# Kernel tuning notes

Hardware: AMD Instinct MI355X
Metric: run time of the kernel (lower is better)

Reference implementation:

```python
import jax, jax.numpy as jnp
import numpy as np

B = 8192          # batch rows
F0 = 2048         # base input features
E = 512           # embed rows added per recursion level
L = 3             # chain depth
OUT = 2048        # MAIN output dim
NNZ_E = 8192      # nnz per embed sparse weight (~16/row)
NNZ_M = 16384     # nnz of MAIN sparse weight (~8/row)


def _spmm_t(rows, cols, vals, x, n_rows):
    """Compute (W_sparse @ x.T).T = x @ W.T for COO W of shape [n_rows, x.shape[1]].
    out[b, r] = sum_{k: rows[k]==r} vals[k] * x[b, cols[k]]
    """
    contrib = x[:, cols] * vals                     # [B, nnz]
    return jax.ops.segment_sum(contrib.T, rows, num_segments=n_rows).T  # [B, n_rows]


def setup_inputs() -> dict:
    key = jax.random.key(0)
    ks = jax.random.split(key, 12)
    widths = [F0, F0 + E, F0 + 2 * E]               # input width at each recursion level
    inp = {"x": jax.random.normal(ks[0], (B, F0), dtype=jnp.float32)}
    for i, w in enumerate(widths):
        inp[f"emb_rows{i}"] = jax.random.randint(ks[1 + 3 * i], (NNZ_E,), 0, E, dtype=jnp.int32)
        inp[f"emb_cols{i}"] = jax.random.randint(ks[2 + 3 * i], (NNZ_E,), 0, w, dtype=jnp.int32)
        inp[f"emb_vals{i}"] = jax.random.normal(ks[3 + 3 * i], (NNZ_E,), dtype=jnp.float32)
    inp["main_rows"] = jax.random.randint(ks[10], (NNZ_M,), 0, OUT, dtype=jnp.int32)
    inp["main_cols"] = jax.random.randint(ks[11], (NNZ_M,), 0, F0 + 3 * E, dtype=jnp.int32)
    inp["main_vals"] = jax.random.normal(jax.random.fold_in(key, 99), (NNZ_M,), dtype=jnp.float32)
    return inp


def reference(x, emb_rows0, emb_cols0, emb_vals0,
              emb_rows1, emb_cols1, emb_vals1,
              emb_rows2, emb_cols2, emb_vals2,
              main_rows, main_cols, main_vals):
    # Recursive chain unrolled oldest-first: each level sparse-mms its embed
    # weight against the running input and concatenates the result.
    h = x
    for rows, cols, vals in ((emb_rows0, emb_cols0, emb_vals0),
                             (emb_rows1, emb_cols1, emb_vals1),
                             (emb_rows2, emb_cols2, emb_vals2)):
        e = _spmm_t(rows, cols, vals, h, E)         # [B, E]
        h = jnp.concatenate([h, e], axis=1)
    # is_last: pass concatenated features through the MAIN sparse linear
    return _spmm_t(main_rows, main_cols, main_vals, h, OUT)  # [B, OUT]
```

## Files before the change

kernel.cpp:

```cpp
#include <hip/hip_runtime.h>
#include <stdint.h>

#define F0    2048
#define EROWS 512
#define NOUT  2048
#define MROWS 8192

typedef __attribute__((ext_vector_type(8))) short bf16x8;
typedef __attribute__((ext_vector_type(4))) float f32x4;
typedef __attribute__((ext_vector_type(8))) unsigned short u16x8;

typedef const __attribute__((address_space(1))) unsigned char ga_t;
typedef __attribute__((address_space(3))) unsigned char lds_t;

__device__ __forceinline__ void async_load16(const void* g, void* l) {
  __builtin_amdgcn_global_load_lds((ga_t*)g, (lds_t*)l, 16, 0, 0);
}

__device__ __forceinline__ unsigned short f2bf(float f) {
  unsigned int u = __builtin_bit_cast(unsigned int, f);
  u += 0x7fffu + ((u >> 16) & 1u);
  return (unsigned short)(u >> 16);
}

__global__ __launch_bounds__(256) void csr_cast_kernel(
    const int* __restrict__ r0, const int* __restrict__ c0, const float* __restrict__ v0, int n0,
    const int* __restrict__ r1, const int* __restrict__ c1, const float* __restrict__ v1, int n1,
    const int* __restrict__ r2, const int* __restrict__ c2, const float* __restrict__ v2, int n2,
    const int* __restrict__ rm, const int* __restrict__ cm, const float* __restrict__ vm, int nm,
    int* __restrict__ rp_all, int* __restrict__ cc_all, float* __restrict__ cv_all)
{
  const int b = blockIdx.x;
  const int tid = threadIdx.x;

  const int* rows; const int* cols; const float* vals; int nnz, nrows;
  if      (b == 0) { rows = r0; cols = c0; vals = v0; nnz = n0; nrows = EROWS; }
  else if (b == 1) { rows = r1; cols = c1; vals = v1; nnz = n1; nrows = EROWS; }
  else if (b == 2) { rows = r2; cols = c2; vals = v2; nnz = n2; nrows = EROWS; }
  else             { rows = rm; cols = cm; vals = vm; nnz = nm; nrows = NOUT; }
  int* rp  = rp_all + b * 4096;
  int* cc  = cc_all + b * 8192;
  float* cv = cv_all + b * 8192;

  __shared__ int hist[NOUT + 1];
  __shared__ int tsum[256];

  for (int i = tid; i < nrows; i += 256) hist[i] = 0;
  __syncthreads();

  int k0 = 0;
  for (; k0 + 2048 <= nnz; k0 += 2048) {
    const int kk = k0 + tid * 8;
    int4 ra = *(const int4*)(rows + kk);
    int4 rb = *(const int4*)(rows + kk + 4);
    atomicAdd(&hist[ra.x], 1); atomicAdd(&hist[ra.y], 1);
    atomicAdd(&hist[ra.z], 1); atomicAdd(&hist[ra.w], 1);
    atomicAdd(&hist[rb.x], 1); atomicAdd(&hist[rb.y], 1);
    atomicAdd(&hist[rb.z], 1); atomicAdd(&hist[rb.w], 1);
  }
  for (int k = k0 + tid; k < nnz; k += 256) atomicAdd(&hist[rows[k]], 1);
  __syncthreads();

  const int per = nrows >> 8;
  const int base = tid * per;
  int sum = 0;
  for (int i = 0; i < per; ++i) sum += hist[base + i];
  tsum[tid] = sum;
  __syncthreads();
  for (int off = 1; off < 256; off <<= 1) {
    int add = (tid >= off) ? tsum[tid - off] : 0;
    __syncthreads();
    tsum[tid] += add;
    __syncthreads();
  }
  int run = (tid == 0) ? 0 : tsum[tid - 1];
  for (int i = 0; i < per; ++i) { int h = hist[base + i]; hist[base + i] = run; run += h; }
  __syncthreads();

  for (int i = tid; i < nrows; i += 256) rp[i] = hist[i];
  if (tid == 0) rp[nrows] = nnz;
  __syncthreads();

  k0 = 0;
  for (; k0 + 2048 <= nnz; k0 += 2048) {
    const int kk = k0 + tid * 8;
    int4   ra = *(const int4*)(rows + kk);
    int4   rb = *(const int4*)(rows + kk + 4);
    int4   ca = *(const int4*)(cols + kk);
    int4   cb2 = *(const int4*)(cols + kk + 4);
    float4 va = *(const float4*)(vals + kk);
    float4 vb = *(const float4*)(vals + kk + 4);
    int p;
    p = atomicAdd(&hist[ra.x], 1); cc[p] = ca.x;  cv[p] = va.x;
    p = atomicAdd(&hist[ra.y], 1); cc[p] = ca.y;  cv[p] = va.y;
    p = atomicAdd(&hist[ra.z], 1); cc[p] = ca.z;  cv[p] = va.z;
    p = atomicAdd(&hist[ra.w], 1); cc[p] = ca.w;  cv[p] = va.w;
    p = atomicAdd(&hist[rb.x], 1); cc[p] = cb2.x; cv[p] = vb.x;
    p = atomicAdd(&hist[rb.y], 1); cc[p] = cb2.y; cv[p] = vb.y;
    p = atomicAdd(&hist[rb.z], 1); cc[p] = cb2.z; cv[p] = vb.z;
    p = atomicAdd(&hist[rb.w], 1); cc[p] = cb2.w; cv[p] = vb.w;
  }
  for (int k = k0 + tid; k < nnz; k += 256) {
    int p = atomicAdd(&hist[rows[k]], 1);
    cc[p] = cols[k]; cv[p] = vals[k];
  }
}

template <bool BF16OUT>
__global__ __launch_bounds__(256) void expand_csr_kernel(
    const int* __restrict__ rp, const int* __restrict__ cc,
    const float* __restrict__ cv, const float* __restrict__ Dsrc,
    void* __restrict__ out, int nrows,
    const float* __restrict__ x, unsigned short* __restrict__ Ab, int cast_base)
{
  const int b = blockIdx.x;
  const int tid = threadIdx.x;

  if (b >= nrows) {
    const int cb = cast_base + (b - nrows);
    const float4* xp = (const float4*)x;
    u16x8* ap = (u16x8*)Ab;
#pragma unroll
    for (int it = 0; it < 4; ++it) {
      int i = cb * 1024 + it * 256 + tid;
      float4 a = xp[2 * i], c = xp[2 * i + 1];
      u16x8 o;
      o[0] = f2bf(a.x); o[1] = f2bf(a.y); o[2] = f2bf(a.z); o[3] = f2bf(a.w);
      o[4] = f2bf(c.x); o[5] = f2bf(c.y); o[6] = f2bf(c.z); o[7] = f2bf(c.w);
      ap[i] = o;
    }
    return;
  }

  const int r = b;
  __shared__ float acc[F0];
  __shared__ int   icol[128];
  __shared__ float ival[128];
  __shared__ int   icnt;

  float4* a4 = (float4*)acc;
  a4[tid * 2]     = (float4){0.f, 0.f, 0.f, 0.f};
  a4[tid * 2 + 1] = (float4){0.f, 0.f, 0.f, 0.f};
  if (tid == 0) icnt = 0;
  __syncthreads();

  const int s = rp[r], e = rp[r + 1];
  for (int i = s + tid; i < e; i += 256) {
    int c = cc[i]; float v = cv[i];
    if (c < F0) atomicAdd(&acc[c], v);
    else { int p = atomicAdd(&icnt, 1); if (p < 128) { icol[p] = c - F0; ival[p] = v; } }
  }
  __syncthreads();
  int n = icnt; if (n > 128) n = 128;

  float4 q0 = a4[tid * 2], q1 = a4[tid * 2 + 1];
  for (int j = 0; j < n; ++j) {
    const float4* src = (const float4*)(Dsrc + (size_t)icol[j] * F0) + tid * 2;
    float v = ival[j];
    float4 s0 = src[0], s1 = src[1];
    q0.x += v * s0.x; q0.y += v * s0.y; q0.z += v * s0.z; q0.w += v * s0.w;
    q1.x += v * s1.x; q1.y += v * s1.y; q1.z += v * s1.z; q1.w += v * s1.w;
  }

  if (BF16OUT) {
    u16x8 o;
    o[0] = f2bf(q0.x); o[1] = f2bf(q0.y); o[2] = f2bf(q0.z); o[3] = f2bf(q0.w);
    o[4] = f2bf(q1.x); o[5] = f2bf(q1.y); o[6] = f2bf(q1.z); o[7] = f2bf(q1.w);
    ((u16x8*)out)[(size_t)r * 256 + tid] = o;
  } else {
    float4* dst = (float4*)out + (size_t)r * 512 + tid * 2;
    dst[0] = q0; dst[1] = q1;
  }
}

__global__ __launch_bounds__(512, 2) void gemm256_kernel(
    const unsigned short* __restrict__ A, const unsigned short* __restrict__ B,
    float* __restrict__ C)
{
  constexpr int K  = F0;
  constexpr int N  = NOUT;
  constexpr int NT = K / 64;

  extern __shared__ __align__(16) unsigned short lds[];
  unsigned short* sA = lds;
  unsigned short* sB = lds + 32768;

  const int tid  = threadIdx.x;
  const int lane = tid & 63;
  const int w    = tid >> 6;
  const int wr   = w >> 2;
  const int wc   = w & 3;
  const int mm   = lane & 15;
  const int g    = lane >> 4;
  const int sx   = mm & 7;
  const int bm   = blockIdx.y;
  const int bn   = blockIdx.x;

  const unsigned short* Ag = A + (size_t)bm * 256 * K;
  const unsigned short* Bg = B + (size_t)bn * 256 * K;

  const int    r0    = tid >> 3;
  const int    c0    = (tid & 7) ^ (r0 & 7);
  const size_t goff0 = (size_t)r0 * K + c0 * 8;
  const size_t goff1 = goff0 + (size_t)64 * K;
  const int    loff0 = tid * 8;
  const int    loff1 = 4096 + tid * 8;

#define STG(Gb, Sb, buf, h, t) do {                                           \
    async_load16((Gb) + goff0 + (size_t)(h) * 128 * K + (t) * 64,             \
                 (Sb) + (buf) * 16384 + (h) * 8192 + loff0);                  \
    async_load16((Gb) + goff1 + (size_t)(h) * 128 * K + (t) * 64,             \
                 (Sb) + (buf) * 16384 + (h) * 8192 + loff1);                  \
  } while (0)

  const unsigned short* paB = sA + (wr * 128 + mm) * 64;
  const unsigned short* pbB = sB + (wc * 64  + mm) * 64;
  const int s0 = ((0 * 4 + g) ^ sx) * 8;
  const int s1 = ((1 * 4 + g) ^ sx) * 8;

  bf16x8 afP[4][2];
  bf16x8 afQ[4][2];
  bf16x8 bf0[2][2];
  bf16x8 bf1[2][2];

#define LDA(dst, buf, qm) do {                                                \
    const unsigned short* p_ = paB + (buf) * 16384 + (qm) * 4096;             \
    _Pragma("unroll") for (int tm = 0; tm < 4; ++tm) {                        \
      dst[tm][0] = *(const bf16x8*)(p_ + tm * 1024 + s0);                     \
      dst[tm][1] = *(const bf16x8*)(p_ + tm * 1024 + s1);                     \
    } } while (0)

#define LDB(dst, buf, qn) do {                                                \
    const unsigned short* p_ = pbB + (buf) * 16384 + (qn) * 2048;             \
    _Pragma("unroll") for (int tn = 0; tn < 2; ++tn) {                        \
      dst[tn][0] = *(const bf16x8*)(p_ + tn * 1024 + s0);                     \
      dst[tn][1] = *(const bf16x8*)(p_ + tn * 1024 + s1);                     \
    } } while (0)

#define MFMA_Q(qm, qn, afX, bfX) do {                                         \
    __builtin_amdgcn_s_setprio(1);                                            \
    _Pragma("unroll") for (int tm = 0; tm < 4; ++tm)                          \
    _Pragma("unroll") for (int tn = 0; tn < 2; ++tn) {                        \
      acc[(qm)*4+tm][(qn)*2+tn] = __builtin_amdgcn_mfma_f32_16x16x32_bf16(    \
          afX[tm][0], bfX[tn][0], acc[(qm)*4+tm][(qn)*2+tn], 0, 0, 0);        \
      acc[(qm)*4+tm][(qn)*2+tn] = __builtin_amdgcn_mfma_f32_16x16x32_bf16(    \
          afX[tm][1], bfX[tn][1], acc[(qm)*4+tm][(qn)*2+tn], 0, 0, 0);        \
    }                                                                         \
    __builtin_amdgcn_s_setprio(0);                                            \
  } while (0)

#define CFENCE     asm volatile("" ::: "memory")
#define BAR        do { CFENCE; __builtin_amdgcn_s_barrier(); CFENCE; } while (0)
#define SCHED0     __builtin_amdgcn_sched_barrier(0)
#define WAIT_VM(n) asm volatile("s_waitcnt vmcnt(" #n ")" ::: "memory")

  f32x4 acc[8][4];
#pragma unroll
  for (int i = 0; i < 8; ++i)
#pragma unroll
    for (int j = 0; j < 4; ++j) acc[i][j] = (f32x4)0.f;

  STG(Bg, sB, 0, 0, 0);
  STG(Bg, sB, 0, 1, 0);
  STG(Ag, sA, 0, 0, 0);
  STG(Ag, sA, 0, 1, 0);
  STG(Bg, sB, 1, 0, 1);
  STG(Bg, sB, 1, 1, 1);
  STG(Ag, sA, 1, 0, 1);
  WAIT_VM(6);
  BAR;
  SCHED0;
  LDA(afP, 0, 0);
  LDB(bf0, 0, 0);

#pragma unroll 2
  for (int t = 0; t < NT; ++t) {
    const int buf  = t & 1;
    const int nbuf = buf ^ 1;

    if (t + 1 < NT) STG(Ag, sA, nbuf, 1, t + 1);
    if (t + 1 < NT) { WAIT_VM(8); } else { WAIT_VM(0); }
    SCHED0;
    LDB(bf1, buf, 1);
    MFMA_Q(0, 0, afP, bf0);

    BAR; SCHED0;
    LDA(afQ, buf, 1);
    MFMA_Q(0, 1, afP, bf1);

    BAR;
    if (t + 2 < NT) STG(Bg, sB, buf, 0, t + 2);
    MFMA_Q(1, 0, afQ, bf0);

    BAR;
    if (t + 2 < NT) {
      STG(Bg, sB, buf, 1, t + 2);
      STG(Ag, sA, buf, 0, t + 2);
      WAIT_VM(6);
      BAR; SCHED0;
      LDA(afP, nbuf, 0);
      LDB(bf0, nbuf, 0);
    } else if (t + 1 < NT) {
      WAIT_VM(0);
      BAR; SCHED0;
      LDA(afP, nbuf, 0);
      LDB(bf0, nbuf, 0);
    }
    MFMA_Q(1, 1, afQ, bf1);
  }

  const int rowb = bm * 256 + wr * 128 + g * 4;
  const int colb = bn * 256 + wc * 64 + mm;
#pragma unroll
  for (int im = 0; im < 8; ++im) {
#pragma unroll
    for (int in2 = 0; in2 < 4; ++in2) {
      const int row = rowb + im * 16;
      const int col = colb + in2 * 16;
#pragma unroll
      for (int r = 0; r < 4; ++r)
        C[(size_t)(row + r) * N + col] = acc[im][in2][r];
    }
  }

#undef STG
#undef LDA
#undef LDB
#undef MFMA_Q
#undef CFENCE
#undef BAR
#undef SCHED0
#undef WAIT_VM
}

extern "C" void kernel_launch(void* const* d_in, const int* in_sizes, int n_in,
                              void* d_out, int out_size, void* d_ws, size_t ws_size,
                              hipStream_t stream)
{
  const float* x   = (const float*)d_in[0];
  const int*   er0 = (const int*)d_in[1];
  const int*   ec0 = (const int*)d_in[2];
  const float* ev0 = (const float*)d_in[3];
  const int*   er1 = (const int*)d_in[4];
  const int*   ec1 = (const int*)d_in[5];
  const float* ev1 = (const float*)d_in[6];
  const int*   er2 = (const int*)d_in[7];
  const int*   ec2 = (const int*)d_in[8];
  const float* ev2 = (const float*)d_in[9];
  const int*   mr  = (const int*)d_in[10];
  const int*   mc  = (const int*)d_in[11];
  const float* mv  = (const float*)d_in[12];
  const int nnz_e0 = in_sizes[1];
  const int nnz_e1 = in_sizes[4];
  const int nnz_e2 = in_sizes[7];
  const int nnz_m  = in_sizes[10];

  int*   rp_all = (int*)d_ws;
  int*   cc_all = rp_all + 4 * 4096;
  float* cv_all = (float*)(cc_all + 48 * 1024);
  float* D      = (float*)(cv_all + 48 * 1024);
  unsigned short* Mb = (unsigned short*)(D + (size_t)3 * EROWS * F0);
  unsigned short* Ab = Mb + (size_t)NOUT * F0;

  hipLaunchKernelGGL(csr_cast_kernel, dim3(4), dim3(256), 0, stream,
                     er0, ec0, ev0, nnz_e0,
                     er1, ec1, ev1, nnz_e1,
                     er2, ec2, ev2, nnz_e2,
                     mr,  mc,  mv,  nnz_m,
                     rp_all, cc_all, cv_all);

  hipLaunchKernelGGL((expand_csr_kernel<false>), dim3(EROWS + 512), dim3(256), 0, stream,
                     rp_all + 0 * 4096, cc_all + 0 * 8192, cv_all + 0 * 8192,
                     D, (void*)D, EROWS, x, Ab, 0);
  hipLaunchKernelGGL((expand_csr_kernel<false>), dim3(EROWS + 512), dim3(256), 0, stream,
                     rp_all + 1 * 4096, cc_all + 1 * 8192, cv_all + 1 * 8192,
                     D, (void*)(D + (size_t)EROWS * F0), EROWS, x, Ab, 512);
  hipLaunchKernelGGL((expand_csr_kernel<false>), dim3(EROWS + 512), dim3(256), 0, stream,
                     rp_all + 2 * 4096, cc_all + 2 * 8192, cv_all + 2 * 8192,
                     D, (void*)(D + (size_t)2 * EROWS * F0), EROWS, x, Ab, 1024);
  hipLaunchKernelGGL((expand_csr_kernel<true>), dim3(NOUT + 512), dim3(256), 0, stream,
                     rp_all + 3 * 4096, cc_all + 3 * 8192, cv_all + 3 * 8192,
                     D, (void*)Mb, NOUT, x, Ab, 1536);

  hipFuncSetAttribute(reinterpret_cast<const void*>(gemm256_kernel),
                      hipFuncAttributeMaxDynamicSharedMemorySize, 131072);
  hipLaunchKernelGGL(gemm256_kernel, dim3(NOUT / 256, MROWS / 256), dim3(512),
                     131072, stream, Ab, Mb, (float*)d_out);
}
```

Measured before the change: 237.3 us.

## Collapse embed chain expansion into a single worklist-driven tree expansion kernel

Replaces the three sequential per-level dense embed-matrix expansions plus the main expansion with one kernel. Each main row walks its references to embed rows through a shared-memory worklist and accumulates directly into the F0-wide row. The x-to-bf16 cast moves into the CSR build kernel, and the GEMM block order is remapped for cache locality. This removes three launches and the D intermediate traffic. The cost is serial worklist processing with a barrier per entry, and a 2048-entry cap that could truncate deep fan-out.

Result: slower. 262.9 us (+10.8%).

```diff
diff --git a/kernel.cpp b/kernel.cpp
--- a/kernel.cpp
+++ b/kernel.cpp
@@ -28,10 +28,27 @@
     const int* __restrict__ r1, const int* __restrict__ c1, const float* __restrict__ v1, int n1,
     const int* __restrict__ r2, const int* __restrict__ c2, const float* __restrict__ v2, int n2,
     const int* __restrict__ rm, const int* __restrict__ cm, const float* __restrict__ vm, int nm,
-    int* __restrict__ rp_all, int* __restrict__ cc_all, float* __restrict__ cv_all)
+    int* __restrict__ rp_all, int* __restrict__ cc_all, float* __restrict__ cv_all,
+    const float* __restrict__ x, unsigned short* __restrict__ Ab)
 {
   const int b = blockIdx.x;
   const int tid = threadIdx.x;
+
+  if (b >= 4) {
+    const int cb = b - 4;
+    const float4* xp = (const float4*)x;
+    u16x8* ap = (u16x8*)Ab;
+#pragma unroll
+    for (int it = 0; it < 4; ++it) {
+      int i = cb * 1024 + it * 256 + tid;
+      float4 a = xp[2 * i], c = xp[2 * i + 1];
+      u16x8 o;
+      o[0] = f2bf(a.x); o[1] = f2bf(a.y); o[2] = f2bf(a.z); o[3] = f2bf(a.w);
+      o[4] = f2bf(c.x); o[5] = f2bf(c.y); o[6] = f2bf(c.z); o[7] = f2bf(c.w);
+      ap[i] = o;
+    }
+    return;
+  }
 
   const int* rows; const int* cols; const float* vals; int nnz, nrows;
   if      (b == 0) { rows = r0; cols = c0; vals = v0; nnz = n0; nrows = EROWS; }
@@ -106,71 +123,62 @@
   }
 }
 
-template <bool BF16OUT>
-__global__ __launch_bounds__(256) void expand_csr_kernel(
-    const int* __restrict__ rp, const int* __restrict__ cc,
-    const float* __restrict__ cv, const float* __restrict__ Dsrc,
-    void* __restrict__ out, int nrows,
-    const float* __restrict__ x, unsigned short* __restrict__ Ab, int cast_base)
+__global__ __launch_bounds__(256) void expand_tree_kernel(
+    const int* __restrict__ rp_all, const int* __restrict__ cc_all,
+    const float* __restrict__ cv_all, unsigned short* __restrict__ Mb)
 {
-  const int b = blockIdx.x;
+  const int r = blockIdx.x;
   const int tid = threadIdx.x;
-
-  if (b >= nrows) {
-    const int cb = cast_base + (b - nrows);
-    const float4* xp = (const float4*)x;
-    u16x8* ap = (u16x8*)Ab;
-#pragma unroll
-    for (int it = 0; it < 4; ++it) {
-      int i = cb * 1024 + it * 256 + tid;
-      float4 a = xp[2 * i], c = xp[2 * i + 1];
-      u16x8 o;
-      o[0] = f2bf(a.x); o[1] = f2bf(a.y); o[2] = f2bf(a.z); o[3] = f2bf(a.w);
-      o[4] = f2bf(c.x); o[5] = f2bf(c.y); o[6] = f2bf(c.z); o[7] = f2bf(c.w);
-      ap[i] = o;
-    }
-    return;
-  }
-
-  const int r = b;
   __shared__ float acc[F0];
-  __shared__ int   icol[128];
-  __shared__ float ival[128];
-  __shared__ int   icnt;
+  __shared__ int   wl_row[2048];
+  __shared__ float wl_sc[2048];
+  __shared__ int   wl_n;
+  __shared__ int   wl_snap;
 
   float4* a4 = (float4*)acc;
   a4[tid * 2]     = (float4){0.f, 0.f, 0.f, 0.f};
   a4[tid * 2 + 1] = (float4){0.f, 0.f, 0.f, 0.f};
-  if (tid == 0) icnt = 0;
-  __syncthreads();
-
-  const int s = rp[r], e = rp[r + 1];
-  for (int i = s + tid; i < e; i += 256) {
-    int c = cc[i]; float v = cv[i];
-    if (c < F0) atomicAdd(&acc[c], v);
-    else { int p = atomicAdd(&icnt, 1); if (p < 128) { icol[p] = c - F0; ival[p] = v; } }
-  }
-  __syncthreads();
-  int n = icnt; if (n > 128) n = 128;
-
-  float4 q0 = a4[tid * 2], q1 = a4[tid * 2 + 1];
-  for (int j = 0; j < n; ++j) {
-    const float4* src = (const float4*)(Dsrc + (size_t)icol[j] * F0) + tid * 2;
-    float v = ival[j];
-    float4 s0 = src[0], s1 = src[1];
-    q0.x += v * s0.x; q0.y += v * s0.y; q0.z += v * s0.z; q0.w += v * s0.w;
-    q1.x += v * s1.x; q1.y += v * s1.y; q1.z += v * s1.z; q1.w += v * s1.w;
-  }
-
-  if (BF16OUT) {
-    u16x8 o;
-    o[0] = f2bf(q0.x); o[1] = f2bf(q0.y); o[2] = f2bf(q0.z); o[3] = f2bf(q0.w);
-    o[4] = f2bf(q1.x); o[5] = f2bf(q1.y); o[6] = f2bf(q1.z); o[7] = f2bf(q1.w);
-    ((u16x8*)out)[(size_t)r * 256 + tid] = o;
-  } else {
-    float4* dst = (float4*)out + (size_t)r * 512 + tid * 2;
-    dst[0] = q0; dst[1] = q1;
-  }
+  if (tid == 0) wl_n = 0;
+  __syncthreads();
+
+  {
+    const int* rp3 = rp_all + 3 * 4096;
+    const int s = rp3[r], e = rp3[r + 1];
+    for (int i = s + tid; i < e; i += 256) {
+      int c = cc_all[3 * 8192 + i]; float v = cv_all[3 * 8192 + i];
+      if (c < F0) atomicAdd(&acc[c], v);
+      else { int p = atomicAdd(&wl_n, 1); if (p < 2048) { wl_row[p] = c - F0; wl_sc[p] = v; } }
+    }
+  }
+  __syncthreads();
+
+  int pos = 0;
+  while (true) {
+    if (tid == 0) wl_snap = wl_n;
+    __syncthreads();
+    int nn = wl_snap;
+    if (nn > 2048) nn = 2048;
+    if (pos >= nn) break;
+    const int   row = wl_row[pos];
+    const float sc  = wl_sc[pos];
+    const int l  = row >> 9;
+    const int lr = row & 511;
+    const int* rp = rp_all + l * 4096;
+    const int s1 = rp[lr], e1 = rp[lr + 1];
+    for (int i = s1 + tid; i < e1; i += 256) {
+      int c = cc_all[l * 8192 + i]; float v = sc * cv_all[l * 8192 + i];
+      if (c < F0) atomicAdd(&acc[c], v);
+      else { int p = atomicAdd(&wl_n, 1); if (p < 2048) { wl_row[p] = c - F0; wl_sc[p] = v; } }
+    }
+    ++pos;
+    __syncthreads();
+  }
+
+  u16x8 o;
+  const float* ap = acc + tid * 8;
+  o[0] = f2bf(ap[0]); o[1] = f2bf(ap[1]); o[2] = f2bf(ap[2]); o[3] = f2bf(ap[3]);
+  o[4] = f2bf(ap[4]); o[5] = f2bf(ap[5]); o[6] = f2bf(ap[6]); o[7] = f2bf(ap[7]);
+  ((u16x8*)Mb)[(size_t)r * 256 + tid] = o;
 }
 
 __global__ __launch_bounds__(512, 2) void gemm256_kernel(
@@ -193,8 +201,11 @@
   const int mm   = lane & 15;
   const int g    = lane >> 4;
   const int sx   = mm & 7;
-  const int bm   = blockIdx.y;
-  const int bn   = blockIdx.x;
+
+  const int flat = blockIdx.y * 8 + blockIdx.x;
+  const int nid  = (flat & 7) * 32 + (flat >> 3);
+  const int bm   = nid >> 3;
+  const int bn   = nid & 7;
 
   const unsigned short* Ag = A + (size_t)bm * 256 * K;
   const unsigned short* Bg = B + (size_t)bn * 256 * K;
@@ -362,25 +373,15 @@
   unsigned short* Mb = (unsigned short*)(D + (size_t)3 * EROWS * F0);
   unsigned short* Ab = Mb + (size_t)NOUT * F0;
 
-  hipLaunchKernelGGL(csr_cast_kernel, dim3(4), dim3(256), 0, stream,
+  hipLaunchKernelGGL(csr_cast_kernel, dim3(4 + 2048), dim3(256), 0, stream,
                      er0, ec0, ev0, nnz_e0,
                      er1, ec1, ev1, nnz_e1,
                      er2, ec2, ev2, nnz_e2,
                      mr,  mc,  mv,  nnz_m,
-                     rp_all, cc_all, cv_all);
-
-  hipLaunchKernelGGL((expand_csr_kernel<false>), dim3(EROWS + 512), dim3(256), 0, stream,
-                     rp_all + 0 * 4096, cc_all + 0 * 8192, cv_all + 0 * 8192,
-                     D, (void*)D, EROWS, x, Ab, 0);
-  hipLaunchKernelGGL((expand_csr_kernel<false>), dim3(EROWS + 512), dim3(256), 0, stream,
-                     rp_all + 1 * 4096, cc_all + 1 * 8192, cv_all + 1 * 8192,
-                     D, (void*)(D + (size_t)EROWS * F0), EROWS, x, Ab, 512);
-  hipLaunchKernelGGL((expand_csr_kernel<false>), dim3(EROWS + 512), dim3(256), 0, stream,
-                     rp_all + 2 * 4096, cc_all + 2 * 8192, cv_all + 2 * 8192,
-                     D, (void*)(D + (size_t)2 * EROWS * F0), EROWS, x, Ab, 1024);
-  hipLaunchKernelGGL((expand_csr_kernel<true>), dim3(NOUT + 512), dim3(256), 0, stream,
-                     rp_all + 3 * 4096, cc_all + 3 * 8192, cv_all + 3 * 8192,
-                     D, (void*)Mb, NOUT, x, Ab, 1536);
+                     rp_all, cc_all, cv_all, x, Ab);
+
+  hipLaunchKernelGGL(expand_tree_kernel, dim3(NOUT), dim3(256), 0, stream,
+                     rp_all, cc_all, cv_all, Mb);
 
   hipFuncSetAttribute(reinterpret_cast<const void*>(gemm256_kernel),
                       hipFuncAttributeMaxDynamicSharedMemorySize, 131072);
```

## Reschedule bf16 GEMM main loop with swizzled block order and quadrant LDS layout

Applied to the files above, without the earlier changes.

Remaps the block index so consecutive workgroups walk along M within a fixed N tile, which should improve L2 reuse of the B operand. Reorganizes the LDS staging so each A/B half covers one compute quadrant. This lets the main loop issue loads, barriers and MFMA quadrants in a new order with partial vmcnt waits. The loop is unrolled in pairs with double-buffered bf0 fragments and the final two tiles peeled, which removes the per-iteration bounds checks. The risks are tighter wait counts that could race, and hardcoded tile counts that tie the code to K=2048.

Result: faster. 227.2 us (-4.3%).

```diff
diff --git a/kernel.cpp b/kernel.cpp
--- a/kernel.cpp
+++ b/kernel.cpp
@@ -193,45 +193,57 @@
   const int mm   = lane & 15;
   const int g    = lane >> 4;
   const int sx   = mm & 7;
-  const int bm   = blockIdx.y;
-  const int bn   = blockIdx.x;
+
+  const int flat = blockIdx.y * 8 + blockIdx.x;
+  const int nid  = (flat & 7) * 32 + (flat >> 3);
+  const int bm   = nid >> 3;
+  const int bn   = nid & 7;
 
   const unsigned short* Ag = A + (size_t)bm * 256 * K;
   const unsigned short* Bg = B + (size_t)bn * 256 * K;
 
   const int    r0    = tid >> 3;
   const int    c0    = (tid & 7) ^ (r0 & 7);
-  const size_t goff0 = (size_t)r0 * K + c0 * 8;
-  const size_t goff1 = goff0 + (size_t)64 * K;
+  const size_t gA0   = (size_t)((r0 & 63) + (r0 >> 6) * 128) * K + c0 * 8;
+  const size_t gB0   = (size_t)((r0 & 31) + (r0 >> 5) * 64)  * K + c0 * 8;
   const int    loff0 = tid * 8;
   const int    loff1 = 4096 + tid * 8;
 
-#define STG(Gb, Sb, buf, h, t) do {                                           \
-    async_load16((Gb) + goff0 + (size_t)(h) * 128 * K + (t) * 64,             \
-                 (Sb) + (buf) * 16384 + (h) * 8192 + loff0);                  \
-    async_load16((Gb) + goff1 + (size_t)(h) * 128 * K + (t) * 64,             \
-                 (Sb) + (buf) * 16384 + (h) * 8192 + loff1);                  \
+#define STG_A(buf, qm, t) do {                                                \
+    async_load16(Ag + gA0 + (size_t)(qm) * 64 * K + (size_t)(t) * 64,         \
+                 sA + (buf) * 16384 + (qm) * 8192 + loff0);                   \
+    async_load16(Ag + gA0 + (size_t)(qm) * 64 * K + (size_t)128 * K +         \
+                 (size_t)(t) * 64,                                            \
+                 sA + (buf) * 16384 + (qm) * 8192 + loff1);                   \
   } while (0)
 
-  const unsigned short* paB = sA + (wr * 128 + mm) * 64;
-  const unsigned short* pbB = sB + (wc * 64  + mm) * 64;
+#define STG_B(buf, qn, t) do {                                                \
+    async_load16(Bg + gB0 + (size_t)(qn) * 32 * K + (size_t)(t) * 64,         \
+                 sB + (buf) * 16384 + (qn) * 8192 + loff0);                   \
+    async_load16(Bg + gB0 + (size_t)(qn) * 32 * K + (size_t)128 * K +         \
+                 (size_t)(t) * 64,                                            \
+                 sB + (buf) * 16384 + (qn) * 8192 + loff1);                   \
+  } while (0)
+
+  const unsigned short* paB = sA + (wr * 64 + mm) * 64;
+  const unsigned short* pbB = sB + (wc * 32 + mm) * 64;
   const int s0 = ((0 * 4 + g) ^ sx) * 8;
   const int s1 = ((1 * 4 + g) ^ sx) * 8;
 
   bf16x8 afP[4][2];
   bf16x8 afQ[4][2];
-  bf16x8 bf0[2][2];
+  bf16x8 bf0A[2][2], bf0B[2][2];
   bf16x8 bf1[2][2];
 
 #define LDA(dst, buf, qm) do {                                                \
-    const unsigned short* p_ = paB + (buf) * 16384 + (qm) * 4096;             \
+    const unsigned short* p_ = paB + (buf) * 16384 + (qm) * 8192;             \
     _Pragma("unroll") for (int tm = 0; tm < 4; ++tm) {                        \
       dst[tm][0] = *(const bf16x8*)(p_ + tm * 1024 + s0);                     \
       dst[tm][1] = *(const bf16x8*)(p_ + tm * 1024 + s1);                     \
     } } while (0)
 
 #define LDB(dst, buf, qn) do {                                                \
-    const unsigned short* p_ = pbB + (buf) * 16384 + (qn) * 2048;             \
+    const unsigned short* p_ = pbB + (buf) * 16384 + (qn) * 8192;             \
     _Pragma("unroll") for (int tn = 0; tn < 2; ++tn) {                        \
       dst[tn][0] = *(const bf16x8*)(p_ + tn * 1024 + s0);                     \
       dst[tn][1] = *(const bf16x8*)(p_ + tn * 1024 + s1);                     \
@@ -260,53 +272,65 @@
 #pragma unroll
     for (int j = 0; j < 4; ++j) acc[i][j] = (f32x4)0.f;
 
-  STG(Bg, sB, 0, 0, 0);
-  STG(Bg, sB, 0, 1, 0);
-  STG(Ag, sA, 0, 0, 0);
-  STG(Ag, sA, 0, 1, 0);
-  STG(Bg, sB, 1, 0, 1);
-  STG(Bg, sB, 1, 1, 1);
-  STG(Ag, sA, 1, 0, 1);
+  STG_B(0, 0, 0); STG_B(0, 1, 0);
+  STG_A(0, 0, 0); STG_A(0, 1, 0);
+  STG_B(1, 0, 1); STG_B(1, 1, 1);
+  STG_A(1, 0, 1);
   WAIT_VM(6);
-  BAR;
-  SCHED0;
+  BAR; SCHED0;
   LDA(afP, 0, 0);
-  LDB(bf0, 0, 0);
-
-#pragma unroll 2
-  for (int t = 0; t < NT; ++t) {
-    const int buf  = t & 1;
-    const int nbuf = buf ^ 1;
-
-    if (t + 1 < NT) STG(Ag, sA, nbuf, 1, t + 1);
-    if (t + 1 < NT) { WAIT_VM(8); } else { WAIT_VM(0); }
-    SCHED0;
-    LDB(bf1, buf, 1);
-    MFMA_Q(0, 0, afP, bf0);
-
-    BAR; SCHED0;
-    LDA(afQ, buf, 1);
+  LDB(bf0A, 0, 0);
+
+#define TILE(buf, nbuf, BF0C, BF0N, t) do {                                   \
+                                                                      \
+    STG_A(nbuf, 1, (t) + 1);                                     \
+    LDB(bf1, buf, 1);                           \
+    MFMA_Q(0, 0, afP, BF0C);                                                  \
+                                                                      \
+    WAIT_VM(8);                                             \
+    BAR; SCHED0;                                                              \
+    LDA(afQ, buf, 1);                                                         \
+    MFMA_Q(0, 1, afP, bf1);                                                   \
+                                                                      \
+    STG_B(buf, 0, (t) + 2);                     \
+    WAIT_VM(2);                                   \
+    BAR; SCHED0;                                                              \
+    LDA(afP, nbuf, 0);                                          \
+    MFMA_Q(1, 1, afQ, bf1);                                                   \
+                                                         \
+    STG_B(buf, 1, (t) + 2);                             \
+    STG_A(buf, 0, (t) + 2);                             \
+    LDB(BF0N, nbuf, 0);                           \
+    MFMA_Q(1, 0, afQ, BF0C);                                                  \
+  } while (0)
+
+  for (int tp = 0; tp < 15; ++tp) {
+    const int t0 = 2 * tp;
+    TILE(0, 1, bf0A, bf0B, t0);
+    TILE(1, 0, bf0B, bf0A, t0 + 1);
+  }
+
+  {
+    STG_A(1, 1, 31);
+    LDB(bf1, 0, 1);
+    MFMA_Q(0, 0, afP, bf0A);
+    WAIT_VM(8); BAR; SCHED0;
+    LDA(afQ, 0, 1);
     MFMA_Q(0, 1, afP, bf1);
-
-    BAR;
-    if (t + 2 < NT) STG(Bg, sB, buf, 0, t + 2);
-    MFMA_Q(1, 0, afQ, bf0);
-
-    BAR;
-    if (t + 2 < NT) {
-      STG(Bg, sB, buf, 1, t + 2);
-      STG(Ag, sA, buf, 0, t + 2);
-      WAIT_VM(6);
-      BAR; SCHED0;
-      LDA(afP, nbuf, 0);
-      LDB(bf0, nbuf, 0);
-    } else if (t + 1 < NT) {
-      WAIT_VM(0);
-      BAR; SCHED0;
-      LDA(afP, nbuf, 0);
-      LDB(bf0, nbuf, 0);
-    }
+    WAIT_VM(2); BAR; SCHED0;
+    LDA(afP, 1, 0);
     MFMA_Q(1, 1, afQ, bf1);
+    LDB(bf0B, 1, 0);
+    MFMA_Q(1, 0, afQ, bf0A);
+  }
+  {
+    LDB(bf1, 1, 1);
+    MFMA_Q(0, 0, afP, bf0B);
+    WAIT_VM(0); BAR; SCHED0;
+    LDA(afQ, 1, 1);
+    MFMA_Q(0, 1, afP, bf1);
+    MFMA_Q(1, 1, afQ, bf1);
+    MFMA_Q(1, 0, afQ, bf0B);
   }
 
   const int rowb = bm * 256 + wr * 128 + g * 4;
@@ -323,10 +347,12 @@
     }
   }
 
-#undef STG
+#undef STG_A
+#undef STG_B
 #undef LDA
 #undef LDB
 #undef MFMA_Q
+#undef TILE
 #undef CFENCE
 #undef BAR
 #undef SCHED0
```
